# Optimization experiments

Hardware: AMD Instinct MI355X
Metric: run time of the kernel (lower is better)

The kernel has to match this reference:

```python
import jax, jax.numpy as jnp
import numpy as np
from jax import lax

BN_EPS = 1e-5

def convbn(x, w, gamma, beta, mean, var):
    # Conv2d(stride=1, padding=1, no bias) + BatchNorm2d in eval mode (fused affine)
    y = lax.conv_general_dilated(x, w, window_strides=(1, 1), padding=((1, 1), (1, 1)),
                                 dimension_numbers=('NCHW', 'OIHW', 'NCHW'))
    inv = gamma / jnp.sqrt(var + BN_EPS)
    return y * inv[None, :, None, None] + (beta - mean * inv)[None, :, None, None]

def affine_scan(z, h, init, axis, reverse):
    # MinGRU recurrence h_i = z_i*_h_i + (1-z_i)*h_{i-1} along `axis` of (B,C,H,W)
    zm = jnp.moveaxis(z, axis, 0)  # (L, B, C, other)
    hm = jnp.moveaxis(h, axis, 0)
    # init: (1, C, 1) broadcasts to (B, C, other)
    carry0 = jnp.broadcast_to(init, zm.shape[1:]).astype(h.dtype)
    def step(carry, zh):
        zt, ht = zh
        new = zt * ht + (1.0 - zt) * carry
        return new, new
    _, out = lax.scan(step, carry0, (zm, hm), reverse=reverse)
    return jnp.moveaxis(out, 0, axis)

def setup_inputs() -> dict:
    key = jax.random.key(0)
    ks = jax.random.split(key, 24)
    B, Cin, Cout, H, W = 4, 64, 64, 256, 256
    C4 = Cout * 4
    d = {}
    d['xs'] = jax.random.normal(ks[0], (B, Cin, H, W), jnp.float32)
    for i, tag in enumerate(['z', 'h', 's']):
        base = 1 + i * 5
        d['w_' + tag] = jax.random.normal(ks[base], (C4, Cin, 3, 3), jnp.float32) * 0.05
        d['g_' + tag] = jax.random.uniform(ks[base + 1], (C4,), jnp.float32, 0.5, 1.5)
        d['b_' + tag] = jax.random.normal(ks[base + 2], (C4,), jnp.float32) * 0.1
        d['m_' + tag] = jax.random.normal(ks[base + 3], (C4,), jnp.float32) * 0.1
        d['v_' + tag] = jax.random.uniform(ks[base + 4], (C4,), jnp.float32, 0.5, 1.5)
    for i, name in enumerate(['h20', 'h21', 'h30', 'h31']):
        d[name] = jnp.zeros((1, Cout, 1), jnp.float32)
    return d

def reference(xs, w_z, g_z, b_z, m_z, v_z, w_h, g_h, b_h, m_h, v_h,
              w_s, g_s, b_s, m_s, v_s, h20, h21, h30, h31):
    B = xs.shape[0]
    zs = jax.nn.sigmoid(convbn(xs, w_z, g_z, b_z, m_z, v_z))
    _hs = convbn(xs, w_h, g_h, b_h, m_h, v_h)
    ss = jax.nn.sigmoid(convbn(xs, w_s, g_s, b_s, m_s, v_s))
    H, W = zs.shape[2], zs.shape[3]
    C = zs.shape[1] // 4
    zs4 = zs.reshape(B, 4, C, H, W)
    _hs4 = _hs.reshape(B, 4, C, H, W)
    ss4 = ss.reshape(B, 4, C, H, W)
    h0 = affine_scan(zs4[:, 0], _hs4[:, 0], h20, axis=2, reverse=False)
    h1 = affine_scan(zs4[:, 1], _hs4[:, 1], h21, axis=2, reverse=True)
    h2 = affine_scan(zs4[:, 2], _hs4[:, 2], h30, axis=3, reverse=False)
    h3 = affine_scan(zs4[:, 3], _hs4[:, 3], h31, axis=3, reverse=True)
    hs = (ss4[:, 0] * h0 + ss4[:, 1] * h1 + ss4[:, 2] * h2 + ss4[:, 3] * h3)
    return hs
```

## Files before the change

### kernel.cpp

```cpp
#include <hip/hip_runtime.h>

typedef _Float16 f16;
typedef _Float16 f16x8 __attribute__((ext_vector_type(8)));
typedef _Float16 f16x4 __attribute__((ext_vector_type(4)));
typedef float    f32x4 __attribute__((ext_vector_type(4)));

#define PIX          65536
#define PACKED_ELEMS 442368
#define XH_ELEMS     16777216

__global__ __launch_bounds__(256) void xcvt_kernel(const float* __restrict__ x, f16* __restrict__ xh)
{
    int i = (blockIdx.x * 256 + threadIdx.x) << 3;
    f32x4 a = *reinterpret_cast<const f32x4*>(x + i);
    f32x4 b = *reinterpret_cast<const f32x4*>(x + i + 4);
    f16x8 o;
#pragma unroll
    for (int j = 0; j < 4; ++j) { o[j] = (f16)a[j]; o[j + 4] = (f16)b[j]; }
    *reinterpret_cast<f16x8*>(xh + i) = o;
}

__global__ void prep_kernel(
    const float* __restrict__ wz, const float* __restrict__ gz, const float* __restrict__ bz,
    const float* __restrict__ mz, const float* __restrict__ vz,
    const float* __restrict__ wh, const float* __restrict__ gh, const float* __restrict__ bh,
    const float* __restrict__ mh, const float* __restrict__ vh,
    const float* __restrict__ wq, const float* __restrict__ gq, const float* __restrict__ bq,
    const float* __restrict__ mq, const float* __restrict__ vq,
    f16* __restrict__ packed, float* __restrict__ bias)
{
    int p = blockIdx.x * 256 + threadIdx.x;
    if (p < PACKED_ELEMS) {
        int i  = p & 7;
        int l  = (p >> 3) & 63;
        int nb = (p >> 9) % 48;
        int kc = (p >> 9) / 48;
        int k  = kc * 32 + ((l >> 4) << 3) + i;
        int n  = (nb << 4) + (l & 15);
        int t  = k >> 6, ci = k & 63;
        int kh = t / 3,  kw = t % 3;
        int arr = n >> 8, co = n & 255;
        const float* w_ = arr == 0 ? wz : arr == 1 ? wh : wq;
        const float* g_ = arr == 0 ? gz : arr == 1 ? gh : gq;
        const float* v_ = arr == 0 ? vz : arr == 1 ? vh : vq;
        float inv = g_[co] / sqrtf(v_[co] + 1e-5f);
        float wv  = w_[((co * 64 + ci) * 3 + kh) * 3 + kw] * inv;
        packed[p] = (f16)wv;
    }
    if (p < 768) {
        int arr = p >> 8, co = p & 255;
        const float* g_ = arr == 0 ? gz : arr == 1 ? gh : gq;
        const float* v_ = arr == 0 ? vz : arr == 1 ? vh : vq;
        const float* b_ = arr == 0 ? bz : arr == 1 ? bh : bq;
        const float* m_ = arr == 0 ? mz : arr == 1 ? mh : mq;
        float inv = g_[co] / sqrtf(v_[co] + 1e-5f);
        bias[p] = b_[co] - m_[co] * inv;
    }
}

__global__ __launch_bounds__(256) void conv_kernel(
    const f16* __restrict__ xh, const f16* __restrict__ Bp, const float* __restrict__ bias,
    f16* __restrict__ Zp, f16* __restrict__ Hp, f16* __restrict__ Sp, int gsel, int b0)
{
    __shared__ f16 As[6 * 34 * 64];
    const int tid  = threadIdx.x;
    const int bid  = blockIdx.x;
    const int a    = bid % 3;
    const int mt   = bid / 3;
    const int bloc = mt >> 9;
    const int b    = b0 + bloc;
    const int rem  = mt & 511;
    const int h0   = (rem >> 3) << 2;
    const int w0   = (rem & 7) << 5;

    for (int idx = tid; idx < 6 * 34 * 64; idx += 256) {
        int wi = idx % 34;
        int r  = idx / 34;
        int hr = r % 6;
        int ci = r / 6;
        int gh2 = h0 - 1 + hr, gw = w0 - 1 + wi;
        f16 v = (f16)0.f;
        if ((unsigned)gh2 < 256u && (unsigned)gw < 256u)
            v = xh[(((b << 6) + ci) << 16) + (gh2 << 8) + gw];
        As[((hr * 34 + wi) << 6) + ((((ci >> 3) ^ (wi & 7)) << 3)) + (ci & 7)] = v;
    }
    __syncthreads();

    const int lane = tid & 63;
    const int wave = tid >> 6;
    const int l15  = lane & 15, l4 = lane >> 4;
    const int wmo  = (wave >> 1) << 6;
    const int nbb  = a * 16 + gsel * 8 + (wave & 1) * 4;

    f32x4 acc[4][4] = {};
    const f16x8* Bv = reinterpret_cast<const f16x8*>(Bp);

    for (int kc = 0; kc < 18; ++kc) {
        const int t   = kc >> 1;
        const int dh  = t / 3, dw = t % 3;
        const int c8  = ((kc & 1) << 2) + l4;
        f16x8 bf[4], af[4];
        const f16x8* bp = Bv + ((kc * 48 + nbb) * 64 + lane);
#pragma unroll
        for (int fn = 0; fn < 4; ++fn) bf[fn] = bp[fn * 64];
#pragma unroll
        for (int fm = 0; fm < 4; ++fm) {
            int p  = wmo + fm * 16 + l15;
            int wi = (p & 31) + dw;
            int hr = (p >> 5) + dh;
            int ai = ((hr * 34 + wi) << 6) + ((c8 ^ (wi & 7)) << 3);
            af[fm] = *reinterpret_cast<const f16x8*>(&As[ai]);
        }
#pragma unroll
        for (int fm = 0; fm < 4; ++fm)
#pragma unroll
            for (int fn = 0; fn < 4; ++fn)
                acc[fm][fn] = __builtin_amdgcn_mfma_f32_16x16x32_f16(af[fm], bf[fn], acc[fm][fn], 0, 0, 0);
    }

    const bool sig = (a != 1);
    f16* arrp = (a == 0 ? Zp : a == 1 ? Hp : Sp);
#pragma unroll
    for (int fn = 0; fn < 4; ++fn) {
        const int col = ((wave & 1) << 6) + (fn << 4) + l15;
        const float bs = bias[a * 256 + gsel * 128 + col];
        const int g2 = col >> 6, c = col & 63;
        f16* base = arrp + ((size_t)(((bloc << 1) + g2) * 64 + c)) * PIX;
#pragma unroll
        for (int fm = 0; fm < 4; ++fm) {
            const int p  = wmo + fm * 16 + (l4 << 2);
            const int hl = p >> 5, wl = p & 31;
            f16x4 pk;
#pragma unroll
            for (int r = 0; r < 4; ++r) {
                float v = acc[fm][fn][r] + bs;
                if (sig) v = 1.f / (1.f + __expf(-v));
                pk[r] = (f16)v;
            }
            __builtin_nontemporal_store(pk,
                reinterpret_cast<f16x4*>(base + ((h0 + hl) << 8) + w0 + wl));
        }
    }
}

__global__ __launch_bounds__(256) void hscan_kernel(
    const f16* __restrict__ Zp, const f16* __restrict__ Hp, const f16* __restrict__ Sp,
    const float* __restrict__ h20, const float* __restrict__ h21, float* __restrict__ out, int b0)
{
    const int w = threadIdx.x;
    const int c = blockIdx.x & 63, bloc = blockIdx.x >> 6;
    const int b = b0 + bloc;
    const size_t g0 = ((size_t)(((bloc << 1) + 0) * 64 + c)) * PIX + w;
    const size_t g1 = ((size_t)(((bloc << 1) + 1) * 64 + c)) * PIX + w;
    const f16 *z0 = Zp + g0, *p0 = Hp + g0, *s0 = Sp + g0;
    const f16 *z1 = Zp + g1, *p1 = Hp + g1, *s1 = Sp + g1;
    float* o = out + ((size_t)(b * 64 + c)) * PIX + w;
    float c0 = h20[c], c1 = h21[c];
#pragma unroll 4
    for (int i = 0; i < 128; ++i) {
        const int rf = i << 8, rb = (255 - i) << 8;
        float zv = (float)__builtin_nontemporal_load(z0 + rf);
        float hv = (float)__builtin_nontemporal_load(p0 + rf);
        float sv = (float)__builtin_nontemporal_load(s0 + rf);
        c0 = fmaf(zv, hv - c0, c0);
        float zw = (float)__builtin_nontemporal_load(z1 + rb);
        float hw = (float)__builtin_nontemporal_load(p1 + rb);
        float sw = (float)__builtin_nontemporal_load(s1 + rb);
        c1 = fmaf(zw, hw - c1, c1);
        o[rf] = sv * c0;
        o[rb] = sw * c1;
    }
#pragma unroll 4
    for (int i = 128; i < 256; ++i) {
        const int rf = i << 8, rb = (255 - i) << 8;
        float zv = (float)__builtin_nontemporal_load(z0 + rf);
        float hv = (float)__builtin_nontemporal_load(p0 + rf);
        float sv = (float)__builtin_nontemporal_load(s0 + rf);
        c0 = fmaf(zv, hv - c0, c0);
        float zw = (float)__builtin_nontemporal_load(z1 + rb);
        float hw = (float)__builtin_nontemporal_load(p1 + rb);
        float sw = (float)__builtin_nontemporal_load(s1 + rb);
        c1 = fmaf(zw, hw - c1, c1);
        o[rf] += sv * c0;
        o[rb] += sw * c1;
    }
}

__global__ __launch_bounds__(256) void wscan_kernel(
    const f16* __restrict__ Zp, const f16* __restrict__ Hp, const f16* __restrict__ Sp,
    const float* __restrict__ h30, const float* __restrict__ h31, float* __restrict__ out, int b0)
{
    const int lane = threadIdx.x & 63;
    const int wid  = (blockIdx.x << 2) + (threadIdx.x >> 6);
    const int hrow = wid & 255, c = (wid >> 8) & 63, bloc = wid >> 14;
    const int b = b0 + bloc;
    const size_t g2 = ((size_t)(((bloc << 1) + 0) * 64 + c)) * PIX + (hrow << 8) + (lane << 2);
    const size_t g3 = ((size_t)(((bloc << 1) + 1) * 64 + c)) * PIX + (hrow << 8) + (lane << 2);
    f16x4 z2 = __builtin_nontemporal_load(reinterpret_cast<const f16x4*>(Zp + g2));
    f16x4 p2 = __builtin_nontemporal_load(reinterpret_cast<const f16x4*>(Hp + g2));
    f16x4 s2 = __builtin_nontemporal_load(reinterpret_cast<const f16x4*>(Sp + g2));
    f16x4 z3 = __builtin_nontemporal_load(reinterpret_cast<const f16x4*>(Zp + g3));
    f16x4 p3 = __builtin_nontemporal_load(reinterpret_cast<const f16x4*>(Hp + g3));
    f16x4 s3 = __builtin_nontemporal_load(reinterpret_cast<const f16x4*>(Sp + g3));

    float a2[4], b2[4], a3[4], b3[4], res[4];
#pragma unroll
    for (int j = 0; j < 4; ++j) {
        float zf = (float)z2[j], hf = (float)p2[j];
        a2[j] = 1.f - zf; b2[j] = zf * hf;
        zf = (float)z3[j]; hf = (float)p3[j];
        a3[j] = 1.f - zf; b3[j] = zf * hf;
    }
    float A = a2[0], Bq = b2[0];
#pragma unroll
    for (int j = 1; j < 4; ++j) { Bq = a2[j] * Bq + b2[j]; A *= a2[j]; }
#pragma unroll
    for (int d = 1; d < 64; d <<= 1) {
        float oA = __shfl_up(A, d), oB = __shfl_up(Bq, d);
        if (lane >= d) { Bq = A * oB + Bq; A = A * oA; }
    }
    {
        float oA = __shfl_up(A, 1), oB = __shfl_up(Bq, 1);
        float xv = h30[c];
        if (lane > 0) xv = oA * xv + oB;
#pragma unroll
        for (int j = 0; j < 4; ++j) { xv = a2[j] * xv + b2[j]; res[j] = (float)s2[j] * xv; }
    }
    A = a3[3]; Bq = b3[3];
#pragma unroll
    for (int j = 2; j >= 0; --j) { Bq = a3[j] * Bq + b3[j]; A *= a3[j]; }
#pragma unroll
    for (int d = 1; d < 64; d <<= 1) {
        float oA = __shfl_down(A, d), oB = __shfl_down(Bq, d);
        if (lane + d < 64) { Bq = A * oB + Bq; A = A * oA; }
    }
    {
        float oA = __shfl_down(A, 1), oB = __shfl_down(Bq, 1);
        float xv = h31[c];
        if (lane < 63) xv = oA * xv + oB;
#pragma unroll
        for (int j = 3; j >= 0; --j) { xv = a3[j] * xv + b3[j]; res[j] += (float)s3[j] * xv; }
    }
    float* op = out + ((size_t)(b * 64 + c)) * PIX + (hrow << 8) + (lane << 2);
    f32x4 prev = *(const f32x4*)op, nv;
#pragma unroll
    for (int j = 0; j < 4; ++j) nv[j] = prev[j] + res[j];
    *(f32x4*)op = nv;
}

extern "C" void kernel_launch(void* const* d_in, const int* in_sizes, int n_in,
                              void* d_out, int out_size, void* d_ws, size_t ws_size,
                              hipStream_t stream)
{
    (void)in_sizes; (void)n_in; (void)out_size;
    const float* xs  = (const float*)d_in[0];
    const float* wz  = (const float*)d_in[1];
    const float* gz  = (const float*)d_in[2];
    const float* bz  = (const float*)d_in[3];
    const float* mz  = (const float*)d_in[4];
    const float* vz  = (const float*)d_in[5];
    const float* wh  = (const float*)d_in[6];
    const float* gh  = (const float*)d_in[7];
    const float* bh  = (const float*)d_in[8];
    const float* mh  = (const float*)d_in[9];
    const float* vh  = (const float*)d_in[10];
    const float* wq  = (const float*)d_in[11];
    const float* gq  = (const float*)d_in[12];
    const float* bq  = (const float*)d_in[13];
    const float* mq  = (const float*)d_in[14];
    const float* vq  = (const float*)d_in[15];
    const float* h20 = (const float*)d_in[16];
    const float* h21 = (const float*)d_in[17];
    const float* h30 = (const float*)d_in[18];
    const float* h31 = (const float*)d_in[19];
    float* out = (float*)d_out;

    char* ws = (char*)d_ws;
    f16*   Bp   = (f16*)ws;
    float* bias = (float*)(ws + 884736);
    f16*   xh   = (f16*)(ws + 884736 + 3072);
    char*  bufs = ws + 884736 + 3072 + (size_t)XH_ELEMS * 2;
    const size_t fixed = 884736 + 3072 + (size_t)XH_ELEMS * 2;

    const size_t per_b = (size_t)3 * 2 * 64 * PIX * 2;
    const int nb = (ws_size >= fixed + 4 * per_b) ? 4
                 : (ws_size >= fixed + 2 * per_b) ? 2 : 1;
    const size_t arr_sz = (size_t)nb * 2 * 64 * PIX * 2;
    f16* Zp = (f16*)bufs;
    f16* Hp = (f16*)(bufs + arr_sz);
    f16* Sp = (f16*)(bufs + 2 * arr_sz);

    xcvt_kernel<<<XH_ELEMS / (256 * 8), 256, 0, stream>>>(xs, xh);
    prep_kernel<<<PACKED_ELEMS / 256, 256, 0, stream>>>(
        wz, gz, bz, mz, vz, wh, gh, bh, mh, vh, wq, gq, bq, mq, vq, Bp, bias);

    for (int b0 = 0; b0 < 4; b0 += nb) {
        conv_kernel<<<nb * 512 * 3, 256, 0, stream>>>(xh, Bp, bias, Zp, Hp, Sp, 0, b0);
        hscan_kernel<<<nb * 64, 256, 0, stream>>>(Zp, Hp, Sp, h20, h21, out, b0);
        conv_kernel<<<nb * 512 * 3, 256, 0, stream>>>(xh, Bp, bias, Zp, Hp, Sp, 1, b0);
        wscan_kernel<<<nb * 4096, 256, 0, stream>>>(Zp, Hp, Sp, h30, h31, out, b0);
    }
}
```

Before: 895.5 us.

## Use padded NHWC fp16 input with direct LDS loads and chunked parallel H-scan

The input is converted to a zero-padded channels-last fp16 layout, so each conv block can fill its shared-memory tile with bulk global_load_lds copies. These replace the per-element gather with its bounds checks. The single sequential H-direction scan (only nb*64 blocks) is replaced by a three-phase chunked scan (chunk summaries, carry propagation, chunk finalize) to expose more parallelism. Conv block IDs are also remapped across groups of 8, likely for XCD locality. The cost is an extra memset of the padded buffer, extra scan launches, and scratch traffic for the chunk summaries.

```diff
diff --git a/kernel.cpp b/kernel.cpp
--- a/kernel.cpp
+++ b/kernel.cpp
@@ -7,17 +7,37 @@
 
 #define PIX          65536
 #define PACKED_ELEMS 442368
-#define XH_ELEMS     16777216
-
-__global__ __launch_bounds__(256) void xcvt_kernel(const float* __restrict__ x, f16* __restrict__ xh)
-{
-    int i = (blockIdx.x * 256 + threadIdx.x) << 3;
-    f32x4 a = *reinterpret_cast<const f32x4*>(x + i);
-    f32x4 b = *reinterpret_cast<const f32x4*>(x + i + 4);
-    f16x8 o;
-#pragma unroll
-    for (int j = 0; j < 4; ++j) { o[j] = (f16)a[j]; o[j + 4] = (f16)b[j]; }
-    *reinterpret_cast<f16x8*>(xh + i) = o;
+#define PADW         258
+#define XHS_BYTES    34080768
+
+__device__ __forceinline__ void gload_lds16(const f16* g, f16* l) {
+    __builtin_amdgcn_global_load_lds(
+        (const __attribute__((address_space(1))) void*)g,
+        (__attribute__((address_space(3))) void*)l, 16, 0, 0);
+}
+
+__global__ __launch_bounds__(256) void xcvt_kernel(const float* __restrict__ x, f16* __restrict__ xh_s)
+{
+    __shared__ f16 t[64][72];
+    const int tid = threadIdx.x;
+    const int wt = blockIdx.x & 3, h = (blockIdx.x >> 2) & 255, b = blockIdx.x >> 10;
+    const int ci = tid >> 2, wq = tid & 3;
+    const float* src = x + (((size_t)((b << 6) + ci)) << 16) + (h << 8) + (wt << 6) + (wq << 4);
+#pragma unroll
+    for (int j4 = 0; j4 < 4; ++j4) {
+        f32x4 v = *reinterpret_cast<const f32x4*>(src + (j4 << 2));
+#pragma unroll
+        for (int jj = 0; jj < 4; ++jj) {
+            int wl = (wq << 4) + (j4 << 2) + jj;
+            int cs = (((ci >> 3) ^ ((1 + wl) & 7)) << 3) + (ci & 7);
+            t[wl][cs] = (f16)v[jj];
+        }
+    }
+    __syncthreads();
+    const int wl = tid >> 2, q = tid & 3;
+    f16* dst = xh_s + (((size_t)b * PADW + (h + 1)) * PADW + (wt << 6) + 1 + wl) * 64 + (q << 4);
+    *reinterpret_cast<f16x8*>(dst)     = *reinterpret_cast<const f16x8*>(&t[wl][(q << 4)]);
+    *reinterpret_cast<f16x8*>(dst + 8) = *reinterpret_cast<const f16x8*>(&t[wl][(q << 4) + 8]);
 }
 
 __global__ void prep_kernel(
@@ -44,8 +64,7 @@
         const float* g_ = arr == 0 ? gz : arr == 1 ? gh : gq;
         const float* v_ = arr == 0 ? vz : arr == 1 ? vh : vq;
         float inv = g_[co] / sqrtf(v_[co] + 1e-5f);
-        float wv  = w_[((co * 64 + ci) * 3 + kh) * 3 + kw] * inv;
-        packed[p] = (f16)wv;
+        packed[p] = (f16)(w_[((co * 64 + ci) * 3 + kh) * 3 + kw] * inv);
     }
     if (p < 768) {
         int arr = p >> 8, co = p & 255;
@@ -59,12 +78,14 @@
 }
 
 __global__ __launch_bounds__(256) void conv_kernel(
-    const f16* __restrict__ xh, const f16* __restrict__ Bp, const float* __restrict__ bias,
-    f16* __restrict__ Zp, f16* __restrict__ Hp, f16* __restrict__ Sp, int gsel, int b0)
+    const f16* __restrict__ xh_s, const f16* __restrict__ Bp, const float* __restrict__ bias,
+    f16* __restrict__ Zp, f16* __restrict__ Hp, f16* __restrict__ Sp,
+    int gsel, int b0, int gdiv8)
 {
     __shared__ f16 As[6 * 34 * 64];
-    const int tid  = threadIdx.x;
-    const int bid  = blockIdx.x;
+    const int tid  = threadIdx.x, lane = tid & 63, wave = tid >> 6;
+    const int raw  = blockIdx.x;
+    const int bid  = (raw & 7) * gdiv8 + (raw >> 3);
     const int a    = bid % 3;
     const int mt   = bid / 3;
     const int bloc = mt >> 9;
@@ -73,42 +94,41 @@
     const int h0   = (rem >> 3) << 2;
     const int w0   = (rem & 7) << 5;
 
-    for (int idx = tid; idx < 6 * 34 * 64; idx += 256) {
-        int wi = idx % 34;
-        int r  = idx / 34;
-        int hr = r % 6;
-        int ci = r / 6;
-        int gh2 = h0 - 1 + hr, gw = w0 - 1 + wi;
-        f16 v = (f16)0.f;
-        if ((unsigned)gh2 < 256u && (unsigned)gw < 256u)
-            v = xh[(((b << 6) + ci) << 16) + (gh2 << 8) + gw];
-        As[((hr * 34 + wi) << 6) + ((((ci >> 3) ^ (wi & 7)) << 3)) + (ci & 7)] = v;
+    {
+        const f16* seg = xh_s + (((size_t)b * PADW + h0) * PADW + w0) * 64;
+#pragma unroll
+        for (int hr = 0; hr < 6; ++hr) {
+            const f16* gh = seg + hr * (PADW * 64);
+            gload_lds16(gh + (tid << 3), &As[hr * 2176 + (wave << 9)]);
+            if (tid < 16)
+                gload_lds16(gh + 2048 + (tid << 3), &As[hr * 2176 + 2048]);
+        }
     }
     __syncthreads();
 
-    const int lane = tid & 63;
-    const int wave = tid >> 6;
-    const int l15  = lane & 15, l4 = lane >> 4;
-    const int wmo  = (wave >> 1) << 6;
-    const int nbb  = a * 16 + gsel * 8 + (wave & 1) * 4;
+    const int l15 = lane & 15, l4 = lane >> 4;
+    const int wmo = (wave >> 1) << 6;
+    const int nbb = a * 16 + gsel * 8 + (wave & 1) * 4;
+    int hl_[4], wl_[4];
+#pragma unroll
+    for (int fm = 0; fm < 4; ++fm) { int p = wmo + fm * 16 + l15; hl_[fm] = p >> 5; wl_[fm] = p & 31; }
 
     f32x4 acc[4][4] = {};
     const f16x8* Bv = reinterpret_cast<const f16x8*>(Bp);
 
+#pragma unroll
     for (int kc = 0; kc < 18; ++kc) {
-        const int t   = kc >> 1;
-        const int dh  = t / 3, dw = t % 3;
-        const int c8  = ((kc & 1) << 2) + l4;
+        const int t  = kc >> 1;
+        const int dh = t / 3, dw = t % 3;
+        const int c8 = ((kc & 1) << 2) + l4;
         f16x8 bf[4], af[4];
-        const f16x8* bp = Bv + ((kc * 48 + nbb) * 64 + lane);
-#pragma unroll
-        for (int fn = 0; fn < 4; ++fn) bf[fn] = bp[fn * 64];
+        const f16x8* bp = Bv + (((kc * 48 + nbb) << 6) + lane);
+#pragma unroll
+        for (int fn = 0; fn < 4; ++fn) bf[fn] = bp[fn << 6];
 #pragma unroll
         for (int fm = 0; fm < 4; ++fm) {
-            int p  = wmo + fm * 16 + l15;
-            int wi = (p & 31) + dw;
-            int hr = (p >> 5) + dh;
-            int ai = ((hr * 34 + wi) << 6) + ((c8 ^ (wi & 7)) << 3);
+            const int wi = wl_[fm] + dw;
+            const int ai = (((hl_[fm] + dh) * 34 + wi) << 6) + ((c8 ^ (wi & 7)) << 3);
             af[fm] = *reinterpret_cast<const f16x8*>(&As[ai]);
         }
 #pragma unroll
@@ -143,46 +163,93 @@
     }
 }
 
-__global__ __launch_bounds__(256) void hscan_kernel(
+__global__ __launch_bounds__(256) void hscanA_kernel(
+    const f16* __restrict__ Zp, const f16* __restrict__ Hp,
+    float* __restrict__ sA0, float* __restrict__ sB0,
+    float* __restrict__ sA1, float* __restrict__ sB1)
+{
+    const int w = threadIdx.x;
+    const int j = blockIdx.x & 7, bcl = blockIdx.x >> 3;
+    const int bloc = bcl >> 6, c = bcl & 63;
+    const f16* z0 = Zp + ((size_t)((bloc * 2 + 0) * 64 + c)) * PIX + w;
+    const f16* p0 = Hp + ((size_t)((bloc * 2 + 0) * 64 + c)) * PIX + w;
+    const f16* z1 = Zp + ((size_t)((bloc * 2 + 1) * 64 + c)) * PIX + w;
+    const f16* p1 = Hp + ((size_t)((bloc * 2 + 1) * 64 + c)) * PIX + w;
+    const int r0 = j << 5;
+    float A0 = 1.f, B0 = 0.f, A1 = 1.f, B1 = 0.f;
+#pragma unroll 8
+    for (int r = 0; r < 32; ++r) {
+        const int rf = (r0 + r) << 8, rb = (r0 + 31 - r) << 8;
+        float z  = (float)__builtin_nontemporal_load(z0 + rf);
+        float hh = (float)__builtin_nontemporal_load(p0 + rf);
+        float a0 = 1.f - z;
+        A0 *= a0; B0 = fmaf(a0, B0, z * hh);
+        float zb = (float)__builtin_nontemporal_load(z1 + rb);
+        float hb = (float)__builtin_nontemporal_load(p1 + rb);
+        float a1 = 1.f - zb;
+        A1 *= a1; B1 = fmaf(a1, B1, zb * hb);
+    }
+    const int idx = (((bcl << 3) + j) << 8) + w;
+    sA0[idx] = A0; sB0[idx] = B0; sA1[idx] = A1; sB1[idx] = B1;
+}
+
+__global__ __launch_bounds__(256) void hscanB_kernel(
+    float* __restrict__ sA0, float* __restrict__ sB0,
+    float* __restrict__ sA1, float* __restrict__ sB1,
+    const float* __restrict__ h20, const float* __restrict__ h21)
+{
+    const int w = threadIdx.x, bcl = blockIdx.x, c = bcl & 63;
+    float cur0 = h20[c];
+#pragma unroll
+    for (int j = 0; j < 8; ++j) {
+        const int idx = (((bcl << 3) + j) << 8) + w;
+        float A = sA0[idx], Bc = sB0[idx];
+        sA0[idx] = cur0;
+        cur0 = fmaf(A, cur0, Bc);
+    }
+    float cur1 = h21[c];
+#pragma unroll
+    for (int j = 7; j >= 0; --j) {
+        const int idx = (((bcl << 3) + j) << 8) + w;
+        float A = sA1[idx], Bc = sB1[idx];
+        sA1[idx] = cur1;
+        cur1 = fmaf(A, cur1, Bc);
+    }
+}
+
+__global__ __launch_bounds__(256) void hscanC_kernel(
     const f16* __restrict__ Zp, const f16* __restrict__ Hp, const f16* __restrict__ Sp,
-    const float* __restrict__ h20, const float* __restrict__ h21, float* __restrict__ out, int b0)
+    const float* __restrict__ st0, const float* __restrict__ st1,
+    float* __restrict__ out, int b0)
 {
     const int w = threadIdx.x;
-    const int c = blockIdx.x & 63, bloc = blockIdx.x >> 6;
-    const int b = b0 + bloc;
-    const size_t g0 = ((size_t)(((bloc << 1) + 0) * 64 + c)) * PIX + w;
-    const size_t g1 = ((size_t)(((bloc << 1) + 1) * 64 + c)) * PIX + w;
-    const f16 *z0 = Zp + g0, *p0 = Hp + g0, *s0 = Sp + g0;
-    const f16 *z1 = Zp + g1, *p1 = Hp + g1, *s1 = Sp + g1;
+    const int j = blockIdx.x & 7, bcl = blockIdx.x >> 3;
+    const int bloc = bcl >> 6, c = bcl & 63, b = b0 + bloc;
+    const size_t gb0 = ((size_t)((bloc * 2 + 0) * 64 + c)) * PIX + w;
+    const size_t gb1 = ((size_t)((bloc * 2 + 1) * 64 + c)) * PIX + w;
+    const int r0 = j << 5;
+    const int idx = (((bcl << 3) + j) << 8) + w;
+    float h1 = st1[idx];
+    float h1b[32];
+#pragma unroll
+    for (int r = 31; r >= 0; --r) {
+        const int row = (r0 + r) << 8;
+        float z  = (float)__builtin_nontemporal_load(Zp + gb1 + row);
+        float hh = (float)__builtin_nontemporal_load(Hp + gb1 + row);
+        h1 = fmaf(z, hh - h1, h1);
+        h1b[r] = h1;
+    }
+    float h0 = st0[idx];
     float* o = out + ((size_t)(b * 64 + c)) * PIX + w;
-    float c0 = h20[c], c1 = h21[c];
-#pragma unroll 4
-    for (int i = 0; i < 128; ++i) {
-        const int rf = i << 8, rb = (255 - i) << 8;
-        float zv = (float)__builtin_nontemporal_load(z0 + rf);
-        float hv = (float)__builtin_nontemporal_load(p0 + rf);
-        float sv = (float)__builtin_nontemporal_load(s0 + rf);
-        c0 = fmaf(zv, hv - c0, c0);
-        float zw = (float)__builtin_nontemporal_load(z1 + rb);
-        float hw = (float)__builtin_nontemporal_load(p1 + rb);
-        float sw = (float)__builtin_nontemporal_load(s1 + rb);
-        c1 = fmaf(zw, hw - c1, c1);
-        o[rf] = sv * c0;
-        o[rb] = sw * c1;
-    }
-#pragma unroll 4
-    for (int i = 128; i < 256; ++i) {
-        const int rf = i << 8, rb = (255 - i) << 8;
-        float zv = (float)__builtin_nontemporal_load(z0 + rf);
-        float hv = (float)__builtin_nontemporal_load(p0 + rf);
-        float sv = (float)__builtin_nontemporal_load(s0 + rf);
-        c0 = fmaf(zv, hv - c0, c0);
-        float zw = (float)__builtin_nontemporal_load(z1 + rb);
-        float hw = (float)__builtin_nontemporal_load(p1 + rb);
-        float sw = (float)__builtin_nontemporal_load(s1 + rb);
-        c1 = fmaf(zw, hw - c1, c1);
-        o[rf] += sv * c0;
-        o[rb] += sw * c1;
+#pragma unroll
+    for (int r = 0; r < 32; ++r) {
+        const int row = (r0 + r) << 8;
+        float z  = (float)__builtin_nontemporal_load(Zp + gb0 + row);
+        float hh = (float)__builtin_nontemporal_load(Hp + gb0 + row);
+        h0 = fmaf(z, hh - h0, h0);
+        float s0 = (float)__builtin_nontemporal_load(Sp + gb0 + row);
+        float s1 = (float)__builtin_nontemporal_load(Sp + gb1 + row);
+        o[row] = s0 * h0 + s1 * h1b[r];
     }
 }
 
@@ -194,8 +261,8 @@
     const int wid  = (blockIdx.x << 2) + (threadIdx.x >> 6);
     const int hrow = wid & 255, c = (wid >> 8) & 63, bloc = wid >> 14;
     const int b = b0 + bloc;
-    const size_t g2 = ((size_t)(((bloc << 1) + 0) * 64 + c)) * PIX + (hrow << 8) + (lane << 2);
-    const size_t g3 = ((size_t)(((bloc << 1) + 1) * 64 + c)) * PIX + (hrow << 8) + (lane << 2);
+    const size_t g2 = ((size_t)((bloc * 2 + 0) * 64 + c)) * PIX + (hrow << 8) + (lane << 2);
+    const size_t g3 = ((size_t)((bloc * 2 + 1) * 64 + c)) * PIX + (hrow << 8) + (lane << 2);
     f16x4 z2 = __builtin_nontemporal_load(reinterpret_cast<const f16x4*>(Zp + g2));
     f16x4 p2 = __builtin_nontemporal_load(reinterpret_cast<const f16x4*>(Hp + g2));
     f16x4 s2 = __builtin_nontemporal_load(reinterpret_cast<const f16x4*>(Sp + g2));
@@ -205,15 +272,15 @@
 
     float a2[4], b2[4], a3[4], b3[4], res[4];
 #pragma unroll
-    for (int j = 0; j < 4; ++j) {
-        float zf = (float)z2[j], hf = (float)p2[j];
-        a2[j] = 1.f - zf; b2[j] = zf * hf;
-        zf = (float)z3[j]; hf = (float)p3[j];
-        a3[j] = 1.f - zf; b3[j] = zf * hf;
+    for (int jj = 0; jj < 4; ++jj) {
+        float zf = (float)z2[jj], hf = (float)p2[jj];
+        a2[jj] = 1.f - zf; b2[jj] = zf * hf;
+        zf = (float)z3[jj]; hf = (float)p3[jj];
+        a3[jj] = 1.f - zf; b3[jj] = zf * hf;
     }
     float A = a2[0], Bq = b2[0];
 #pragma unroll
-    for (int j = 1; j < 4; ++j) { Bq = a2[j] * Bq + b2[j]; A *= a2[j]; }
+    for (int jj = 1; jj < 4; ++jj) { Bq = a2[jj] * Bq + b2[jj]; A *= a2[jj]; }
 #pragma unroll
     for (int d = 1; d < 64; d <<= 1) {
         float oA = __shfl_up(A, d), oB = __shfl_up(Bq, d);
@@ -224,11 +291,11 @@
         float xv = h30[c];
         if (lane > 0) xv = oA * xv + oB;
 #pragma unroll
-        for (int j = 0; j < 4; ++j) { xv = a2[j] * xv + b2[j]; res[j] = (float)s2[j] * xv; }
+        for (int jj = 0; jj < 4; ++jj) { xv = a2[jj] * xv + b2[jj]; res[jj] = (float)s2[jj] * xv; }
     }
     A = a3[3]; Bq = b3[3];
 #pragma unroll
-    for (int j = 2; j >= 0; --j) { Bq = a3[j] * Bq + b3[j]; A *= a3[j]; }
+    for (int jj = 2; jj >= 0; --jj) { Bq = a3[jj] * Bq + b3[jj]; A *= a3[jj]; }
 #pragma unroll
     for (int d = 1; d < 64; d <<= 1) {
         float oA = __shfl_down(A, d), oB = __shfl_down(Bq, d);
@@ -239,12 +306,12 @@
         float xv = h31[c];
         if (lane < 63) xv = oA * xv + oB;
 #pragma unroll
-        for (int j = 3; j >= 0; --j) { xv = a3[j] * xv + b3[j]; res[j] += (float)s3[j] * xv; }
+        for (int jj = 3; jj >= 0; --jj) { xv = a3[jj] * xv + b3[jj]; res[jj] += (float)s3[jj] * xv; }
     }
     float* op = out + ((size_t)(b * 64 + c)) * PIX + (hrow << 8) + (lane << 2);
     f32x4 prev = *(const f32x4*)op, nv;
 #pragma unroll
-    for (int j = 0; j < 4; ++j) nv[j] = prev[j] + res[j];
+    for (int jj = 0; jj < 4; ++jj) nv[jj] = prev[jj] + res[jj];
     *(f32x4*)op = nv;
 }
 
@@ -278,26 +345,34 @@
     char* ws = (char*)d_ws;
     f16*   Bp   = (f16*)ws;
     float* bias = (float*)(ws + 884736);
-    f16*   xh   = (f16*)(ws + 884736 + 3072);
-    char*  bufs = ws + 884736 + 3072 + (size_t)XH_ELEMS * 2;
-    const size_t fixed = 884736 + 3072 + (size_t)XH_ELEMS * 2;
-
-    const size_t per_b = (size_t)3 * 2 * 64 * PIX * 2;
+    f16*   xh_s = (f16*)(ws + 887808);
+    const size_t fixed = 887808 + (size_t)XHS_BYTES;
+
+    const size_t per_b = 2097152 + 50331648;
     const int nb = (ws_size >= fixed + 4 * per_b) ? 4
                  : (ws_size >= fixed + 2 * per_b) ? 2 : 1;
+    float* sums = (float*)(ws + fixed);
+    const size_t SUMN = (size_t)nb * 131072;
+    float* sA0 = sums;            float* sB0 = sums + SUMN;
+    float* sA1 = sums + 2 * SUMN; float* sB1 = sums + 3 * SUMN;
+    char*  bufs = ws + fixed + (size_t)nb * 2097152;
     const size_t arr_sz = (size_t)nb * 2 * 64 * PIX * 2;
     f16* Zp = (f16*)bufs;
     f16* Hp = (f16*)(bufs + arr_sz);
     f16* Sp = (f16*)(bufs + 2 * arr_sz);
 
-    xcvt_kernel<<<XH_ELEMS / (256 * 8), 256, 0, stream>>>(xs, xh);
+    hipMemsetAsync(xh_s, 0, XHS_BYTES, stream);
+    xcvt_kernel<<<4096, 256, 0, stream>>>(xs, xh_s);
     prep_kernel<<<PACKED_ELEMS / 256, 256, 0, stream>>>(
         wz, gz, bz, mz, vz, wh, gh, bh, mh, vh, wq, gq, bq, mq, vq, Bp, bias);
 
+    const int cgrid = nb * 512 * 3;
     for (int b0 = 0; b0 < 4; b0 += nb) {
-        conv_kernel<<<nb * 512 * 3, 256, 0, stream>>>(xh, Bp, bias, Zp, Hp, Sp, 0, b0);
-        hscan_kernel<<<nb * 64, 256, 0, stream>>>(Zp, Hp, Sp, h20, h21, out, b0);
-        conv_kernel<<<nb * 512 * 3, 256, 0, stream>>>(xh, Bp, bias, Zp, Hp, Sp, 1, b0);
+        conv_kernel<<<cgrid, 256, 0, stream>>>(xh_s, Bp, bias, Zp, Hp, Sp, 0, b0, cgrid / 8);
+        hscanA_kernel<<<nb * 64 * 8, 256, 0, stream>>>(Zp, Hp, sA0, sB0, sA1, sB1);
+        hscanB_kernel<<<nb * 64, 256, 0, stream>>>(sA0, sB0, sA1, sB1, h20, h21);
+        hscanC_kernel<<<nb * 64 * 8, 256, 0, stream>>>(Zp, Hp, Sp, sA0, sA1, out, b0);
+        conv_kernel<<<cgrid, 256, 0, stream>>>(xh_s, Bp, bias, Zp, Hp, Sp, 1, b0, cgrid / 8);
         wscan_kernel<<<nb * 4096, 256, 0, stream>>>(Zp, Hp, Sp, h30, h31, out, b0);
     }
 }
```

After: 750.7 us. -16.2%, faster.
